# Kernel tuning notes

Hardware: AMD Instinct MI355X
Metric: run time of the kernel (lower is better)

The kernel has to match this reference:

```python
import jax, jax.numpy as jnp
import numpy as np

D = 512      # d_encoder
H = 8        # num_attn_heads
DH = 64      # d_attn
B = 8
S = 1024


def setup_inputs() -> dict:
    key = jax.random.key(0)
    ks = jax.random.split(key, 12)
    lim_in = 1.0 / np.sqrt(D)
    inp = {
        "Q": jax.random.normal(ks[0], (B, S, D), dtype=jnp.float32),
        "K": jax.random.normal(ks[1], (B, S, D), dtype=jnp.float32),
        "V": jax.random.normal(ks[2], (B, S, D), dtype=jnp.float32),
        # per-head projection weights stacked over heads: [H, D, DH]
        "Wq": jax.random.uniform(ks[3], (H, D, DH), jnp.float32, -lim_in, lim_in),
        "bq": jax.random.uniform(ks[4], (H, DH), jnp.float32, -lim_in, lim_in),
        "Wk": jax.random.uniform(ks[5], (H, D, DH), jnp.float32, -lim_in, lim_in),
        "bk": jax.random.uniform(ks[6], (H, DH), jnp.float32, -lim_in, lim_in),
        "Wv": jax.random.uniform(ks[7], (H, D, DH), jnp.float32, -lim_in, lim_in),
        "bv": jax.random.uniform(ks[8], (H, DH), jnp.float32, -lim_in, lim_in),
        "Wo": jax.random.uniform(ks[9], (D, D), jnp.float32, -lim_in, lim_in),
        "bo": jax.random.uniform(ks[10], (D,), jnp.float32, -lim_in, lim_in),
    }
    return inp


def reference(Q, K, V, Wq, bq, Wk, bk, Wv, bv, Wo, bo):
    scale = 1.0 / np.sqrt(DH).astype(np.float32)
    # per-head projections (the torch loop over heads, batched): [B,H,S,DH]
    Qh = jnp.einsum("bsd,hde->bhse", Q, Wq) + bq[None, :, None, :]
    Kh = jnp.einsum("bsd,hde->bhse", K, Wk) + bk[None, :, None, :]
    Vh = jnp.einsum("bsd,hde->bhse", V, Wv) + bv[None, :, None, :]
    # scaled dot-product attention with materialized scores [B,H,S,S]
    scores = jnp.einsum("bhse,bhte->bhst", Qh, Kh) * scale
    probs = jax.nn.softmax(scores, axis=-1)
    x = jnp.einsum("bhst,bhte->bhse", probs, Vh)  # [B,H,S,DH]
    # NOTE: original torch code does x.view(B, S, H*DH) directly on the
    # (B,H,S,DH) contiguous tensor WITHOUT transposing heads/time; we
    # faithfully replicate that memory-layout reshape.
    x = x.reshape(B, S, H * DH)
    x = x @ Wo + bo
    # dropout p=0.0 (p_drop set to 0 for deterministic reference)
    return x
```

## Files before the change

### kernel.cpp

```cpp
#include <hip/hip_runtime.h>
#include <hip/hip_bf16.h>

#define D_ENC 512
#define NH 8
#define DHD 64
#define BB 8
#define SS 1024

typedef unsigned short u16;
typedef __attribute__((ext_vector_type(8))) short short8;
typedef __attribute__((ext_vector_type(4))) float floatx4;

__device__ inline u16 f2bf(float f) {
    __hip_bfloat16 h = __float2bfloat16(f);
    return *reinterpret_cast<u16*>(&h);
}

__device__ inline void glds16(const u16* g, u16* l) {
    __builtin_amdgcn_global_load_lds(
        (const __attribute__((address_space(1))) void*)g,
        (__attribute__((address_space(3))) void*)l, 16, 0, 0);
}

__global__ __launch_bounds__(256) void prep_all(
    const float* __restrict__ Wq, const float* __restrict__ Wk,
    const float* __restrict__ Wv, const float* __restrict__ Wo,
    const float* __restrict__ Q, const float* __restrict__ K,
    const float* __restrict__ V,
    u16* __restrict__ WqT, u16* __restrict__ WkT, u16* __restrict__ WvT,
    u16* __restrict__ WoT, u16* __restrict__ Xbf)
{
    int bx = blockIdx.x;
    if (bx < 4096) {
        int tid = bx * 256 + threadIdx.x;
        const int WSZ = NH * D_ENC * DHD;
        if (tid < 3 * WSZ) {
            int wi = tid / WSZ, r = tid % WSZ;
            int d = r & 511;
            int e = (r >> 9) & 63;
            int h = r >> 15;
            const float* src = wi == 0 ? Wq : (wi == 1 ? Wk : Wv);
            u16* dst = wi == 0 ? WqT : (wi == 1 ? WkT : WvT);
            dst[r] = f2bf(src[h * (D_ENC * DHD) + d * DHD + e]);
        } else {
            int r = tid - 3 * WSZ;
            int d = r & 511, n = r >> 9;
            WoT[r] = f2bf(Wo[d * D_ENC + n]);
        }
    } else {
        int t = (bx - 4096) * 256 + threadIdx.x;
        int p = t / 524288, i = t % 524288;
        const float* src = p == 0 ? Q : (p == 1 ? K : V);
        const float4* s4 = reinterpret_cast<const float4*>(src) + (size_t)i * 2;
        float4 a = s4[0], b = s4[1];
        u16 hv[8] = { f2bf(a.x), f2bf(a.y), f2bf(a.z), f2bf(a.w),
                      f2bf(b.x), f2bf(b.y), f2bf(b.z), f2bf(b.w) };
        *reinterpret_cast<uint4*>(Xbf + (size_t)t * 8) =
            *reinterpret_cast<const uint4*>(hv);
    }
}

__global__ __launch_bounds__(256, 4) void qkv_gemm(
    const u16* __restrict__ Xbf,
    const u16* __restrict__ WqT, const u16* __restrict__ WkT,
    const u16* __restrict__ WvT,
    const float* __restrict__ bq, const float* __restrict__ bk,
    const float* __restrict__ bv,
    u16* __restrict__ Qh, u16* __restrict__ Kh, u16* __restrict__ VhT)
{
    const int proj = blockIdx.z;
    const u16* X = Xbf + (size_t)proj * (BB * SS * D_ENC);
    const u16* WT = proj == 0 ? WqT : (proj == 1 ? WkT : WvT);
    const float* bias = proj == 0 ? bq : (proj == 1 ? bk : bv);
    u16* out = proj == 0 ? Qh : (proj == 1 ? Kh : VhT);
    const float oscale = proj == 0 ? 0.125f : 1.0f;

    const int m0 = blockIdx.x * 128;
    const int n0 = blockIdx.y * 64;
    __shared__ __align__(16) char smem[(128 * 64 + 64 * 64) * 2];
    u16* As = (u16*)smem;
    u16* Bs = As + 128 * 64;
    u16* Ts = (u16*)smem;

    const int tid = threadIdx.x, lane = tid & 63, w = tid >> 6;
    const int q = lane >> 4, l15 = lane & 15;
    const int lr = lane >> 3;
    const int lc = (lane & 7) ^ (lr & 7);

    floatx4 acc[2][4] = {};

    for (int d0 = 0; d0 < D_ENC; d0 += 64) {
        #pragma unroll
        for (int j = 0; j < 4; ++j) {
            int r = (j * 4 + w) * 8 + lr;
            glds16(X + (size_t)(m0 + r) * D_ENC + d0 + lc * 8,
                   As + (j * 4 + w) * 512);
        }
        #pragma unroll
        for (int j = 0; j < 2; ++j) {
            int r = (j * 4 + w) * 8 + lr;
            glds16(WT + (size_t)(n0 + r) * D_ENC + d0 + lc * 8,
                   Bs + (j * 4 + w) * 512);
        }
        __syncthreads();
        #pragma unroll
        for (int ks = 0; ks < 2; ++ks) {
            const int co = ((ks * 4 + q) ^ (l15 & 7)) * 8;
            short8 a0 = *(const short8*)&As[(32 * w + l15) * 64 + co];
            short8 a1 = *(const short8*)&As[(32 * w + 16 + l15) * 64 + co];
            #pragma unroll
            for (int f = 0; f < 4; ++f) {
                short8 bf = *(const short8*)&Bs[(f * 16 + l15) * 64 + co];
                acc[0][f] = __builtin_amdgcn_mfma_f32_16x16x32_bf16(a0, bf, acc[0][f], 0, 0, 0);
                acc[1][f] = __builtin_amdgcn_mfma_f32_16x16x32_bf16(a1, bf, acc[1][f], 0, 0, 0);
            }
        }
        __syncthreads();
    }

    const int b = m0 >> 10, sb = m0 & 1023, h = n0 >> 6;
    if (proj < 2) {
        u16* dst = out + ((size_t)(b * NH + h) * SS + sb) * DHD;
        #pragma unroll
        for (int i = 0; i < 2; ++i)
            #pragma unroll
            for (int f = 0; f < 4; ++f) {
                float bv_ = bias[n0 + f * 16 + l15];
                #pragma unroll
                for (int r = 0; r < 4; ++r)
                    dst[(32 * w + 16 * i + q * 4 + r) * DHD + f * 16 + l15] =
                        f2bf((acc[i][f][r] + bv_) * oscale);
            }
    } else {
        #pragma unroll
        for (int i = 0; i < 2; ++i)
            #pragma unroll
            for (int f = 0; f < 4; ++f) {
                float bv_ = bias[n0 + f * 16 + l15];
                #pragma unroll
                for (int r = 0; r < 4; ++r)
                    Ts[(f * 16 + l15) * 136 + 32 * w + 16 * i + q * 4 + r] =
                        f2bf(acc[i][f][r] + bv_);
            }
        __syncthreads();
        u16* dst = out + (size_t)(b * NH + h) * DHD * SS + sb;
        #pragma unroll
        for (int p2 = 0; p2 < 4; ++p2) {
            int c = (tid + 256 * p2) * 8;
            int e = c >> 7, s = c & 127;
            uint4 v = *(const uint4*)&Ts[e * 136 + s];
            *(uint4*)&dst[(size_t)e * SS + s] = v;
        }
    }
}

__global__ __launch_bounds__(256, 4) void flash_attn(
    const u16* __restrict__ Qh, const u16* __restrict__ Kh,
    const u16* __restrict__ VhT, u16* __restrict__ Xb)
{
    const int s0 = blockIdx.x * 64;
    const int h = blockIdx.y, b = blockIdx.z;
    const size_t bh = (size_t)(b * NH + h);

    __shared__ __align__(16) u16 Ks[2][64 * 64], Vs[2][64 * 64], Ps[64 * 64];

    const int tid = threadIdx.x, lane = tid & 63, w = tid >> 6;
    const int q = lane >> 4, l15 = lane & 15;
    const int lr = lane >> 3, lc = (lane & 7) ^ (lr & 7);

    const u16* qrow = Qh + (bh * SS + s0 + 16 * w + l15) * DHD;
    short8 qb0 = *(const short8*)(qrow + q * 8);
    short8 qb1 = *(const short8*)(qrow + 32 + q * 8);

    const u16* kbase = Kh + bh * SS * DHD;
    const u16* vbase = VhT + bh * DHD * SS;

    #pragma unroll
    for (int j = 0; j < 2; ++j) {
        int r = (j * 4 + w) * 8 + lr;
        glds16(kbase + (size_t)r * DHD + lc * 8, Ks[0] + (j * 4 + w) * 512);
        glds16(vbase + (size_t)r * SS + lc * 8, Vs[0] + (j * 4 + w) * 512);
    }

    floatx4 O[4] = {};
    floatx4 L = {0.f, 0.f, 0.f, 0.f};
    const short8 ones = {16256, 16256, 16256, 16256,
                         16256, 16256, 16256, 16256};

    for (int kt = 0; kt < SS / 64; ++kt) {
        __syncthreads();
        if (kt + 1 < SS / 64) {
            const int k1 = (kt + 1) * 64;
            u16* kd = Ks[(kt + 1) & 1];
            u16* vd = Vs[(kt + 1) & 1];
            #pragma unroll
            for (int j = 0; j < 2; ++j) {
                int r = (j * 4 + w) * 8 + lr;
                glds16(kbase + (size_t)(k1 + r) * DHD + lc * 8,
                       kd + (j * 4 + w) * 512);
                glds16(vbase + (size_t)r * SS + k1 + lc * 8,
                       vd + (j * 4 + w) * 512);
            }
        }
        const u16* ks_ = Ks[kt & 1];
        const u16* vs_ = Vs[kt & 1];

        floatx4 sacc[4] = {};
        #pragma unroll
        for (int f = 0; f < 4; ++f) {
            const int co0 = ((0 * 4 + q) ^ (l15 & 7)) * 8;
            const int co1 = ((1 * 4 + q) ^ (l15 & 7)) * 8;
            short8 ka0 = *(const short8*)&ks_[(f * 16 + l15) * 64 + co0];
            short8 ka1 = *(const short8*)&ks_[(f * 16 + l15) * 64 + co1];
            sacc[f] = __builtin_amdgcn_mfma_f32_16x16x32_bf16(ka0, qb0, sacc[f], 0, 0, 0);
            sacc[f] = __builtin_amdgcn_mfma_f32_16x16x32_bf16(ka1, qb1, sacc[f], 0, 0, 0);
        }

        #pragma unroll
        for (int f = 0; f < 4; ++f) {
            ushort4 pk;
            pk.x = f2bf(__expf(sacc[f][0]));
            pk.y = f2bf(__expf(sacc[f][1]));
            pk.z = f2bf(__expf(sacc[f][2]));
            pk.w = f2bf(__expf(sacc[f][3]));
            const int chunk = (2 * f + (q >> 1)) ^ (l15 & 7);
            *(ushort4*)&Ps[(16 * w + l15) * 64 + chunk * 8 + (q & 1) * 4] = pk;
        }

        #pragma unroll
        for (int ks = 0; ks < 2; ++ks) {
            const int co = ((ks * 4 + q) ^ (l15 & 7)) * 8;
            short8 pa = *(const short8*)&Ps[(16 * w + l15) * 64 + co];
            L = __builtin_amdgcn_mfma_f32_16x16x32_bf16(pa, ones, L, 0, 0, 0);
            #pragma unroll
            for (int f = 0; f < 4; ++f) {
                short8 vb = *(const short8*)&vs_[(f * 16 + l15) * 64 + co];
                O[f] = __builtin_amdgcn_mfma_f32_16x16x32_bf16(pa, vb, O[f], 0, 0, 0);
            }
        }
    }

    u16* dst = Xb + (bh * SS + s0) * DHD;
    #pragma unroll
    for (int f = 0; f < 4; ++f)
        #pragma unroll
        for (int r = 0; r < 4; ++r)
            dst[(16 * w + q * 4 + r) * DHD + f * 16 + l15] =
                f2bf(O[f][r] / L[r]);
}

__global__ __launch_bounds__(256, 4) void out_gemm(
    const u16* __restrict__ X, const u16* __restrict__ WT,
    const float* __restrict__ bias, float* __restrict__ out)
{
    const int m0 = blockIdx.x * 128;
    const int n0 = blockIdx.y * 64;
    __shared__ __align__(16) u16 As[128 * 64];
    __shared__ __align__(16) u16 Bs[64 * 64];

    const int tid = threadIdx.x, lane = tid & 63, w = tid >> 6;
    const int q = lane >> 4, l15 = lane & 15;
    const int lr = lane >> 3, lc = (lane & 7) ^ (lr & 7);

    floatx4 acc[2][4] = {};

    for (int d0 = 0; d0 < D_ENC; d0 += 64) {
        #pragma unroll
        for (int j = 0; j < 4; ++j) {
            int r = (j * 4 + w) * 8 + lr;
            glds16(X + (size_t)(m0 + r) * D_ENC + d0 + lc * 8,
                   As + (j * 4 + w) * 512);
        }
        #pragma unroll
        for (int j = 0; j < 2; ++j) {
            int r = (j * 4 + w) * 8 + lr;
            glds16(WT + (size_t)(n0 + r) * D_ENC + d0 + lc * 8,
                   Bs + (j * 4 + w) * 512);
        }
        __syncthreads();
        #pragma unroll
        for (int ks = 0; ks < 2; ++ks) {
            const int co = ((ks * 4 + q) ^ (l15 & 7)) * 8;
            short8 a0 = *(const short8*)&As[(32 * w + l15) * 64 + co];
            short8 a1 = *(const short8*)&As[(32 * w + 16 + l15) * 64 + co];
            #pragma unroll
            for (int f = 0; f < 4; ++f) {
                short8 bf = *(const short8*)&Bs[(f * 16 + l15) * 64 + co];
                acc[0][f] = __builtin_amdgcn_mfma_f32_16x16x32_bf16(a0, bf, acc[0][f], 0, 0, 0);
                acc[1][f] = __builtin_amdgcn_mfma_f32_16x16x32_bf16(a1, bf, acc[1][f], 0, 0, 0);
            }
        }
        __syncthreads();
    }
    #pragma unroll
    for (int i = 0; i < 2; ++i)
        #pragma unroll
        for (int f = 0; f < 4; ++f) {
            float bv_ = bias[n0 + f * 16 + l15];
            #pragma unroll
            for (int r = 0; r < 4; ++r)
                out[(size_t)(m0 + 32 * w + 16 * i + q * 4 + r) * D_ENC +
                    n0 + f * 16 + l15] = acc[i][f][r] + bv_;
        }
}

extern "C" void kernel_launch(void* const* d_in, const int* in_sizes, int n_in,
                              void* d_out, int out_size, void* d_ws, size_t ws_size,
                              hipStream_t stream)
{
    const float* Q  = (const float*)d_in[0];
    const float* K  = (const float*)d_in[1];
    const float* V  = (const float*)d_in[2];
    const float* Wq = (const float*)d_in[3];
    const float* bq = (const float*)d_in[4];
    const float* Wk = (const float*)d_in[5];
    const float* bk = (const float*)d_in[6];
    const float* Wv = (const float*)d_in[7];
    const float* bv = (const float*)d_in[8];
    const float* Wo = (const float*)d_in[9];
    const float* bo = (const float*)d_in[10];
    float* out = (float*)d_out;

    char* ws = (char*)d_ws;
    u16* WqT = (u16*)(ws + 0);
    u16* WkT = (u16*)(ws + 524288);
    u16* WvT = (u16*)(ws + 1048576);
    u16* WoT = (u16*)(ws + 1572864);
    u16* Xbf = (u16*)(ws + 2097152);
    u16* Xb  = (u16*)(ws + 2097152);
    u16* Qh  = (u16*)(ws + 27262976);
    u16* Kh  = (u16*)(ws + 35651584);
    u16* VhT = (u16*)(ws + 44040192);

    hipLaunchKernelGGL(prep_all, dim3(10240), dim3(256), 0, stream,
                       Wq, Wk, Wv, Wo, Q, K, V, WqT, WkT, WvT, WoT, Xbf);
    hipLaunchKernelGGL(qkv_gemm, dim3(64, 8, 3), dim3(256), 0, stream,
                       Xbf, WqT, WkT, WvT, bq, bk, bv, Qh, Kh, VhT);
    hipLaunchKernelGGL(flash_attn, dim3(16, 8, 8), dim3(256), 0, stream,
                       Qh, Kh, VhT, Xb);
    hipLaunchKernelGGL(out_gemm, dim3(64, 8), dim3(256), 0, stream,
                       Xb, WoT, bo, out);
}
```

Baseline: 173.6 us.

## Widen QKV GEMM tile to 128x128 and fold log2e into Q scale for exp2

The QKV projection GEMM now uses 128x128 output tiles with a 2x2 wave layout and 4x4 MFMA accumulators per wave, halving the grid in N. This doubles operand reuse from LDS and cuts redundant loads of X. The V-transpose epilogue is adapted to write two heads per block. Separately, the Q scale absorbs log2(e) so the attention softmax can use exp2f instead of __expf. The larger tile raises register pressure, so launch bounds drop to 3 blocks per SM.

```diff
diff --git a/kernel.cpp b/kernel.cpp
--- a/kernel.cpp
+++ b/kernel.cpp
@@ -10,6 +10,8 @@
 typedef unsigned short u16;
 typedef __attribute__((ext_vector_type(8))) short short8;
 typedef __attribute__((ext_vector_type(4))) float floatx4;
+
+#define QSCALE 0.18033688011112042f
 
 __device__ inline u16 f2bf(float f) {
     __hip_bfloat16 h = __float2bfloat16(f);
@@ -60,7 +62,7 @@
     }
 }
 
-__global__ __launch_bounds__(256, 4) void qkv_gemm(
+__global__ __launch_bounds__(256, 3) void qkv_gemm(
     const u16* __restrict__ Xbf,
     const u16* __restrict__ WqT, const u16* __restrict__ WkT,
     const u16* __restrict__ WvT,
@@ -73,21 +75,22 @@
     const u16* WT = proj == 0 ? WqT : (proj == 1 ? WkT : WvT);
     const float* bias = proj == 0 ? bq : (proj == 1 ? bk : bv);
     u16* out = proj == 0 ? Qh : (proj == 1 ? Kh : VhT);
-    const float oscale = proj == 0 ? 0.125f : 1.0f;
+    const float oscale = proj == 0 ? QSCALE : 1.0f;
 
     const int m0 = blockIdx.x * 128;
-    const int n0 = blockIdx.y * 64;
-    __shared__ __align__(16) char smem[(128 * 64 + 64 * 64) * 2];
+    const int n0 = blockIdx.y * 128;
+    __shared__ __align__(16) char smem[128 * 136 * 2];
     u16* As = (u16*)smem;
     u16* Bs = As + 128 * 64;
     u16* Ts = (u16*)smem;
 
     const int tid = threadIdx.x, lane = tid & 63, w = tid >> 6;
+    const int wm = w & 1, wn = w >> 1;
     const int q = lane >> 4, l15 = lane & 15;
     const int lr = lane >> 3;
     const int lc = (lane & 7) ^ (lr & 7);
 
-    floatx4 acc[2][4] = {};
+    floatx4 acc[4][4] = {};
 
     for (int d0 = 0; d0 < D_ENC; d0 += 64) {
         #pragma unroll
@@ -95,10 +98,6 @@
             int r = (j * 4 + w) * 8 + lr;
             glds16(X + (size_t)(m0 + r) * D_ENC + d0 + lc * 8,
                    As + (j * 4 + w) * 512);
-        }
-        #pragma unroll
-        for (int j = 0; j < 2; ++j) {
-            int r = (j * 4 + w) * 8 + lr;
             glds16(WT + (size_t)(n0 + r) * D_ENC + d0 + lc * 8,
                    Bs + (j * 4 + w) * 512);
         }
@@ -106,50 +105,60 @@
         #pragma unroll
         for (int ks = 0; ks < 2; ++ks) {
             const int co = ((ks * 4 + q) ^ (l15 & 7)) * 8;
-            short8 a0 = *(const short8*)&As[(32 * w + l15) * 64 + co];
-            short8 a1 = *(const short8*)&As[(32 * w + 16 + l15) * 64 + co];
+            short8 a[4], bb[4];
+            #pragma unroll
+            for (int i = 0; i < 4; ++i)
+                a[i] = *(const short8*)&As[(64 * wm + 16 * i + l15) * 64 + co];
+            #pragma unroll
+            for (int f = 0; f < 4; ++f)
+                bb[f] = *(const short8*)&Bs[(64 * wn + 16 * f + l15) * 64 + co];
+            #pragma unroll
+            for (int i = 0; i < 4; ++i)
+                #pragma unroll
+                for (int f = 0; f < 4; ++f)
+                    acc[i][f] = __builtin_amdgcn_mfma_f32_16x16x32_bf16(
+                        a[i], bb[f], acc[i][f], 0, 0, 0);
+        }
+        __syncthreads();
+    }
+
+    const int b = m0 >> 10, sb = m0 & 1023;
+    if (proj < 2) {
+        const int h = blockIdx.y * 2 + wn;
+        u16* dst = out + ((size_t)(b * NH + h) * SS + sb) * DHD;
+        #pragma unroll
+        for (int i = 0; i < 4; ++i)
             #pragma unroll
             for (int f = 0; f < 4; ++f) {
-                short8 bf = *(const short8*)&Bs[(f * 16 + l15) * 64 + co];
-                acc[0][f] = __builtin_amdgcn_mfma_f32_16x16x32_bf16(a0, bf, acc[0][f], 0, 0, 0);
-                acc[1][f] = __builtin_amdgcn_mfma_f32_16x16x32_bf16(a1, bf, acc[1][f], 0, 0, 0);
-            }
-        }
-        __syncthreads();
-    }
-
-    const int b = m0 >> 10, sb = m0 & 1023, h = n0 >> 6;
-    if (proj < 2) {
-        u16* dst = out + ((size_t)(b * NH + h) * SS + sb) * DHD;
-        #pragma unroll
-        for (int i = 0; i < 2; ++i)
-            #pragma unroll
-            for (int f = 0; f < 4; ++f) {
-                float bv_ = bias[n0 + f * 16 + l15];
+                float bv_ = bias[n0 + wn * 64 + f * 16 + l15];
                 #pragma unroll
                 for (int r = 0; r < 4; ++r)
-                    dst[(32 * w + 16 * i + q * 4 + r) * DHD + f * 16 + l15] =
+                    dst[(64 * wm + 16 * i + q * 4 + r) * DHD + f * 16 + l15] =
                         f2bf((acc[i][f][r] + bv_) * oscale);
             }
     } else {
         #pragma unroll
-        for (int i = 0; i < 2; ++i)
+        for (int i = 0; i < 4; ++i)
             #pragma unroll
             for (int f = 0; f < 4; ++f) {
-                float bv_ = bias[n0 + f * 16 + l15];
-                #pragma unroll
-                for (int r = 0; r < 4; ++r)
-                    Ts[(f * 16 + l15) * 136 + 32 * w + 16 * i + q * 4 + r] =
-                        f2bf(acc[i][f][r] + bv_);
-            }
-        __syncthreads();
-        u16* dst = out + (size_t)(b * NH + h) * DHD * SS + sb;
-        #pragma unroll
-        for (int p2 = 0; p2 < 4; ++p2) {
+                float bv_ = bias[n0 + wn * 64 + f * 16 + l15];
+                ushort4 pk;
+                pk.x = f2bf(acc[i][f][0] + bv_);
+                pk.y = f2bf(acc[i][f][1] + bv_);
+                pk.z = f2bf(acc[i][f][2] + bv_);
+                pk.w = f2bf(acc[i][f][3] + bv_);
+                *(ushort4*)&Ts[(wn * 64 + f * 16 + l15) * 136 +
+                               wm * 64 + i * 16 + q * 4] = pk;
+            }
+        __syncthreads();
+        #pragma unroll
+        for (int p2 = 0; p2 < 8; ++p2) {
             int c = (tid + 256 * p2) * 8;
             int e = c >> 7, s = c & 127;
             uint4 v = *(const uint4*)&Ts[e * 136 + s];
-            *(uint4*)&dst[(size_t)e * SS + s] = v;
+            const int h = blockIdx.y * 2 + (e >> 6);
+            *(uint4*)&out[(size_t)(b * NH + h) * DHD * SS +
+                          (size_t)(e & 63) * SS + sb + s] = v;
         }
     }
 }
@@ -208,8 +217,8 @@
         floatx4 sacc[4] = {};
         #pragma unroll
         for (int f = 0; f < 4; ++f) {
-            const int co0 = ((0 * 4 + q) ^ (l15 & 7)) * 8;
-            const int co1 = ((1 * 4 + q) ^ (l15 & 7)) * 8;
+            const int co0 = (q ^ (l15 & 7)) * 8;
+            const int co1 = ((4 + q) ^ (l15 & 7)) * 8;
             short8 ka0 = *(const short8*)&ks_[(f * 16 + l15) * 64 + co0];
             short8 ka1 = *(const short8*)&ks_[(f * 16 + l15) * 64 + co1];
             sacc[f] = __builtin_amdgcn_mfma_f32_16x16x32_bf16(ka0, qb0, sacc[f], 0, 0, 0);
@@ -219,10 +228,10 @@
         #pragma unroll
         for (int f = 0; f < 4; ++f) {
             ushort4 pk;
-            pk.x = f2bf(__expf(sacc[f][0]));
-            pk.y = f2bf(__expf(sacc[f][1]));
-            pk.z = f2bf(__expf(sacc[f][2]));
-            pk.w = f2bf(__expf(sacc[f][3]));
+            pk.x = f2bf(exp2f(sacc[f][0]));
+            pk.y = f2bf(exp2f(sacc[f][1]));
+            pk.z = f2bf(exp2f(sacc[f][2]));
+            pk.w = f2bf(exp2f(sacc[f][3]));
             const int chunk = (2 * f + (q >> 1)) ^ (l15 & 7);
             *(ushort4*)&Ps[(16 * w + l15) * 64 + chunk * 8 + (q & 1) * 4] = pk;
         }
@@ -334,7 +343,7 @@
 
     hipLaunchKernelGGL(prep_all, dim3(10240), dim3(256), 0, stream,
                        Wq, Wk, Wv, Wo, Q, K, V, WqT, WkT, WvT, WoT, Xbf);
-    hipLaunchKernelGGL(qkv_gemm, dim3(64, 8, 3), dim3(256), 0, stream,
+    hipLaunchKernelGGL(qkv_gemm, dim3(64, 4, 3), dim3(256), 0, stream,
                        Xbf, WqT, WkT, WvT, bq, bk, bv, Qh, Kh, VhT);
     hipLaunchKernelGGL(flash_attn, dim3(16, 8, 8), dim3(256), 0, stream,
                        Qh, Kh, VhT, Xb);
```

Measured after the change: 177.4 us. +2.2%, slower.
